# Optimization experiments

Measured on AMD Instinct MI355X. Metric: run time of the kernel, lower is better.

## Reference

```python
import jax, jax.numpy as jnp
import numpy as np

N_NODES = 100000
N_EDGES = 600000
IN_FEAT = 128
OUT_FEAT = 128
REL_NUM = 5


def setup_inputs() -> dict:
    key = jax.random.key(0)
    k = jax.random.split(key, 7)
    h = jax.random.normal(k[0], (N_NODES, IN_FEAT), dtype=jnp.float32)
    weight = jax.random.normal(k[1], (REL_NUM, IN_FEAT, OUT_FEAT), dtype=jnp.float32)
    W_0 = jax.random.normal(k[2], (IN_FEAT, OUT_FEAT), dtype=jnp.float32)
    norm = jax.random.uniform(k[3], (N_EDGES,), dtype=jnp.float32)
    src = jax.random.randint(k[4], (N_EDGES,), 0, N_NODES, dtype=jnp.int32)
    dst = jax.random.randint(k[5], (N_EDGES,), 0, N_NODES, dtype=jnp.int32)
    edge_id = jax.random.randint(k[6], (N_EDGES,), 0, REL_NUM, dtype=jnp.int32)
    return {"h": h, "weight": weight, "W_0": W_0, "norm": norm,
            "src": src, "dst": dst, "edge_id": edge_id}


def reference(h, weight, W_0, norm, src, dst, edge_id):
    # Per-edge msg = h[src] @ weight[edge_id] * norm.
    # Equivalent, efficient form: transform all nodes by every relation weight
    # once (R is small), then gather per edge instead of materializing an
    # [E, in, out] weight tensor.
    all_h = jnp.einsum('ni,rio->rno', h, weight)          # [R, N, out]
    msg = all_h[edge_id, src] * norm[:, None]             # [E, out]
    h_sum = jax.ops.segment_sum(msg, dst, num_segments=h.shape[0])  # [N, out]
    out = jax.nn.relu(h @ W_0 + h_sum)                    # [N, out]
    return out
```

## Files before the change

kernel.cpp:

```cpp
#include <hip/hip_runtime.h>
#include <hip/hip_bf16.h>


#define NN   100000
#define NE   600000
#define FEAT 128
#define RNUM 5
#define CAP  32
#define KC   24

#define SCAT_B 2344
#define BT_B   384

typedef __attribute__((ext_vector_type(8))) short short8;
typedef __attribute__((ext_vector_type(4))) float float4v;

static __device__ __forceinline__ unsigned short f2bf(float x) {
  union { float f; unsigned u; } v; v.f = x;
  unsigned r = v.u + 0x7FFFu + ((v.u >> 16) & 1u);
  return (unsigned short)(r >> 16);
}

__global__ void k_prep(const int* __restrict__ src, const int* __restrict__ dst,
                       const int* __restrict__ eid, const float* __restrict__ norm,
                       const float* __restrict__ weight, const float* __restrict__ W0,
                       int* __restrict__ cnt, int2* __restrict__ s_edge,
                       unsigned short* __restrict__ Bt) {
  int bid = blockIdx.x;
  if (bid < SCAT_B) {
    int e = bid * 256 + threadIdx.x;
    if (e < NE) {
      int d = dst[e];
      int p = atomicAdd(&cnt[d], 1);
      if (p < CAP) {
        union { float f; int i; } nb; nb.f = norm[e];
        s_edge[(size_t)d * CAP + p] = make_int2(src[e] | (eid[e] << 20), nb.i);
      }
    }
  } else {
    int u = (bid - SCAT_B) * 256 + threadIdx.x;
    if (u < FEAT * KC * 32) {
      int j = u & 7, g = u >> 3;
      int ln = g & 63, n0 = (g >> 6) & 7, c = g >> 9;
      int o = n0 * 16 + (ln & 15);
      int k = c * 32 + ((ln >> 4) << 3) + j;
      float v = (k < 640) ? weight[(k >> 7) * 16384 + (k & 127) * 128 + o]
                          : W0[(k - 640) * 128 + o];
      Bt[u] = f2bf(v);
    }
  }
}

static __device__ __forceinline__ void accum_edge(float acc[RNUM][4], int ex,
                                                  int ey, float4v v) {
  union { int i; float f; } nb; nb.i = ey;
  int r = ex >> 20;
  float nm[RNUM];
#pragma unroll
  for (int rr = 0; rr < RNUM; ++rr) nm[rr] = (r == rr) ? nb.f : 0.f;
#pragma unroll
  for (int rr = 0; rr < RNUM; ++rr)
#pragma unroll
    for (int i = 0; i < 4; ++i) acc[rr][i] += nm[rr] * v[i];
}

__global__ __launch_bounds__(512, 6) void k_fused(
    const float* __restrict__ h, const int* __restrict__ cnt,
    const int2* __restrict__ s_edge, const unsigned short* __restrict__ Bt,
    float* __restrict__ out) {
  __shared__ uint4 Atile[2 * KC * 64];
  int tid = threadIdx.x;
  int wv = tid >> 6, lane = tid & 63;
  int base = blockIdx.x * 32;
  uint4* Aw = Atile + (wv >> 2) * (KC * 64);
  uint2* Aw2 = (uint2*)Aw;
  const float4v* hf4 = (const float4v*)h;

  int g2 = lane >> 5, t2 = lane & 31;
  int cB = t2 >> 3, kk = (t2 >> 1) & 3, par = t2 & 1;
#pragma unroll 1
  for (int pp = 0; pp < 2; ++pp) {
    int node = base + wv * 4 + pp * 2 + g2;
    int row = (wv & 3) * 4 + pp * 2 + g2;
    int glen = cnt[node]; if (glen > CAP) glen = CAP;
    const int4* ep4 = (const int4*)(s_edge + (size_t)node * CAP);
    float4v idf = hf4[(size_t)node * 32 + t2];
    float acc[RNUM][4] = {};
    int npair = glen >> 1;
    int4 d = (glen > 0) ? ep4[0] : make_int4(0, 0, 0, 0);
    for (int p = 0; p < npair; ++p) {
      int4 dn = ep4[p + 1];
      float4v v0 = hf4[(size_t)(d.x & 0xFFFFF) * 32 + t2];
      float4v v1 = hf4[(size_t)(d.z & 0xFFFFF) * 32 + t2];
      accum_edge(acc, d.x, d.y, v0);
      accum_edge(acc, d.z, d.w, v1);
      d = dn;
    }
    if (glen & 1) {
      float4v v = hf4[(size_t)(d.x & 0xFFFFF) * 32 + t2];
      accum_edge(acc, d.x, d.y, v);
    }
#pragma unroll
    for (int rr = 0; rr < RNUM; ++rr) {
      int c = rr * 4 + cB;
      uint2 pk;
      pk.x = (unsigned)f2bf(acc[rr][0]) | ((unsigned)f2bf(acc[rr][1]) << 16);
      pk.y = (unsigned)f2bf(acc[rr][2]) | ((unsigned)f2bf(acc[rr][3]) << 16);
      int sidx = c * 64 + kk * 16 + (row ^ ((c * 4 + kk) & 7));
      Aw2[sidx * 2 + par] = pk;
    }
    {
      int c = 20 + cB;
      uint2 idv;
      idv.x = (unsigned)f2bf(idf[0]) | ((unsigned)f2bf(idf[1]) << 16);
      idv.y = (unsigned)f2bf(idf[2]) | ((unsigned)f2bf(idf[3]) << 16);
      int sidx = c * 64 + kk * 16 + (row ^ ((c * 4 + kk) & 7));
      Aw2[sidx * 2 + par] = idv;
    }
  }
  __syncthreads();

  int m = lane & 15, qq = lane >> 4;
  float4v cacc[2];
  cacc[0] = (float4v){0.f, 0.f, 0.f, 0.f};
  cacc[1] = (float4v){0.f, 0.f, 0.f, 0.f};
#pragma unroll
  for (int c = 0; c < KC; ++c) {
    int sx = qq * 16 + (m ^ ((c * 4 + qq) & 7));
    short8 af0 = *(const short8*)&Atile[c * 64 + sx];
    short8 af1 = *(const short8*)&Atile[KC * 64 + c * 64 + sx];
    short8 bf  = *(const short8*)&Bt[((c * 8 + wv) * 64 + lane) * 8];
    cacc[0] = __builtin_amdgcn_mfma_f32_16x16x32_bf16(af0, bf, cacc[0], 0, 0, 0);
    cacc[1] = __builtin_amdgcn_mfma_f32_16x16x32_bf16(af1, bf, cacc[1], 0, 0, 0);
  }

  __syncthreads();
  float* Cs = (float*)Atile;
#pragma unroll
  for (int tt = 0; tt < 2; ++tt)
#pragma unroll
    for (int r = 0; r < 4; ++r) {
      float v = cacc[tt][r];
      Cs[(tt * 16 + qq * 4 + r) * 132 + wv * 16 + m] = v > 0.f ? v : 0.f;
    }
  __syncthreads();
  int r0 = tid >> 4, c0 = (tid & 15) * 8;
  float4v w0 = *(const float4v*)&Cs[r0 * 132 + c0];
  float4v w1 = *(const float4v*)&Cs[r0 * 132 + c0 + 4];
  float* op = out + (size_t)(base + r0) * FEAT + c0;
  *(float4v*)op = w0;
  *(float4v*)(op + 4) = w1;
}

__global__ void k_slow_mm(const float* __restrict__ h, const float* __restrict__ W0,
                          float* __restrict__ out) {
  __shared__ float hn[128];
  int n = blockIdx.x, t = threadIdx.x;
  hn[t] = h[(size_t)n * 128 + t];
  __syncthreads();
  float a = 0.f;
  for (int i = 0; i < 128; ++i) a += hn[i] * W0[i * 128 + t];
  out[(size_t)n * 128 + t] = a;
}
__global__ void k_slow_edge(const float* __restrict__ h, const float* __restrict__ weight,
                            const float* __restrict__ norm, const int* __restrict__ src,
                            const int* __restrict__ dst, const int* __restrict__ eid,
                            float* __restrict__ out) {
  __shared__ float hs[128];
  int e = blockIdx.x, t = threadIdx.x;
  hs[t] = h[(size_t)src[e] * 128 + t];
  __syncthreads();
  const float* W = weight + (size_t)eid[e] * 16384;
  float a = 0.f;
  for (int i = 0; i < 128; ++i) a += hs[i] * W[i * 128 + t];
  atomicAdd(&out[(size_t)dst[e] * 128 + t], a * norm[e]);
}
__global__ void k_slow_relu(float* out) {
  int i = blockIdx.x * 256 + threadIdx.x;
  if (i < NN * FEAT) out[i] = fmaxf(out[i], 0.f);
}

extern "C" void kernel_launch(void* const* d_in, const int* in_sizes, int n_in,
                              void* d_out, int out_size, void* d_ws, size_t ws_size,
                              hipStream_t stream) {
  const float* h      = (const float*)d_in[0];
  const float* weight = (const float*)d_in[1];
  const float* W0     = (const float*)d_in[2];
  const float* norm   = (const float*)d_in[3];
  const int*   src    = (const int*)d_in[4];
  const int*   dst    = (const int*)d_in[5];
  const int*   eid    = (const int*)d_in[6];
  float* out = (float*)d_out;

  char* ws = (char*)d_ws;
  size_t off = 0;
  auto wsalloc = [&](size_t bytes) -> char* {
    char* p = ws + off;
    off += (bytes + 255) & ~(size_t)255;
    return p;
  };
  unsigned short* Bt  = (unsigned short*)wsalloc((size_t)FEAT * KC * 32 * 2);
  int*   cnt      = (int*)wsalloc((size_t)NN * 4);
  int2*  s_edge   = (int2*)wsalloc((size_t)NN * CAP * 8 + 256);

  if (ws_size >= off) {
    hipMemsetAsync(cnt, 0, (size_t)NN * 4, stream);
    k_prep <<<SCAT_B + BT_B, 256, 0, stream>>>(src, dst, eid, norm, weight,
                                               W0, cnt, s_edge, Bt);
    k_fused<<<NN / 32, 512, 0, stream>>>(h, cnt, s_edge, Bt, out);
  } else {
    k_slow_mm  <<<NN, 128, 0, stream>>>(h, W0, out);
    k_slow_edge<<<NE, 128, 0, stream>>>(h, weight, norm, src, dst, eid, out);
    k_slow_relu<<<(NN * FEAT + 255) / 256, 256, 0, stream>>>(out);
  }
}
```

Measured before the change: 203.8 us.

## Fuse memset, prep and fused compute into one cooperative persistent kernel

Replaces the memset plus two launches with a single cooperative kernel. It zeroes the counters and fills the weight tile, then does a grid sync, the edge scatter, another grid sync, and finally processes node tiles through a persistent loop driven by an atomic tile counter. The aim is to remove launch gaps and kernel-boundary drains, at the cost of two grid-wide barriers and a lower occupancy bound (4 waves per SIMD instead of 6) with a fixed 512-block grid. If the cooperative launch fails, it falls back to the old path.

```diff
diff --git a/kernel.cpp b/kernel.cpp
--- a/kernel.cpp
+++ b/kernel.cpp
@@ -1,5 +1,6 @@
 #include <hip/hip_runtime.h>
 #include <hip/hip_bf16.h>
+#include <hip/hip_cooperative_groups.h>
 
 
 #define NN   100000
@@ -8,6 +9,9 @@
 #define RNUM 5
 #define CAP  32
 #define KC   24
+#define NTILE (NN / 32)
+#define CGRID 512
+#define GSTRIDE (CGRID * 512)
 
 #define SCAT_B 2344
 #define BT_B   384
@@ -19,6 +23,149 @@
   union { float f; unsigned u; } v; v.f = x;
   unsigned r = v.u + 0x7FFFu + ((v.u >> 16) & 1u);
   return (unsigned short)(r >> 16);
+}
+
+static __device__ __forceinline__ void bt_fill(int u, const float* __restrict__ weight,
+                                               const float* __restrict__ W0,
+                                               unsigned short* __restrict__ Bt) {
+  int j = u & 7, g = u >> 3;
+  int ln = g & 63, n0 = (g >> 6) & 7, c = g >> 9;
+  int o = n0 * 16 + (ln & 15);
+  int k = c * 32 + ((ln >> 4) << 3) + j;
+  float v = (k < 640) ? weight[(k >> 7) * 16384 + (k & 127) * 128 + o]
+                      : W0[(k - 640) * 128 + o];
+  Bt[u] = f2bf(v);
+}
+
+static __device__ __forceinline__ void accum_edge(float acc[RNUM][4], int ex,
+                                                  int ey, float4v v) {
+  union { int i; float f; } nb; nb.i = ey;
+  int r = ex >> 20;
+  float nm[RNUM];
+#pragma unroll
+  for (int rr = 0; rr < RNUM; ++rr) nm[rr] = (r == rr) ? nb.f : 0.f;
+#pragma unroll
+  for (int rr = 0; rr < RNUM; ++rr)
+#pragma unroll
+    for (int i = 0; i < 4; ++i) acc[rr][i] += nm[rr] * v[i];
+}
+
+__global__ __launch_bounds__(512, 4) void k_all(
+    const float* __restrict__ h, const int* __restrict__ src,
+    const int* __restrict__ dst, const int* __restrict__ eid,
+    const float* __restrict__ norm, const float* __restrict__ weight,
+    const float* __restrict__ W0, int* __restrict__ cnt,
+    int2* __restrict__ s_edge, unsigned short* __restrict__ Bt,
+    float* __restrict__ out) {
+  namespace cg = cooperative_groups;
+  cg::grid_group grid = cg::this_grid();
+  __shared__ uint4 Atile[2 * KC * 64];
+  __shared__ int tsh;
+  int tid = threadIdx.x;
+  int gtid = blockIdx.x * 512 + tid;
+
+  if (gtid <= NN) cnt[gtid] = 0;
+  if (gtid < FEAT * KC * 32) bt_fill(gtid, weight, W0, Bt);
+  grid.sync();
+
+  for (int e = gtid; e < NE; e += GSTRIDE) {
+    int d = dst[e];
+    int p = atomicAdd(&cnt[d], 1);
+    if (p < CAP) {
+      union { float f; int i; } nb; nb.f = norm[e];
+      s_edge[(size_t)d * CAP + p] = make_int2(src[e] | (eid[e] << 20), nb.i);
+    }
+  }
+  grid.sync();
+
+  int wv = tid >> 6, lane = tid & 63;
+  int g2 = lane >> 5, t2 = lane & 31;
+  int cB = t2 >> 3, kk = (t2 >> 1) & 3, par = t2 & 1;
+  int m = lane & 15, qq = lane >> 4;
+  uint4* Aw = Atile + (wv >> 2) * (KC * 64);
+  uint2* Aw2 = (uint2*)Aw;
+  const float4v* hf4 = (const float4v*)h;
+
+  for (;;) {
+    __syncthreads();
+    if (tid == 0) tsh = atomicAdd(&cnt[NN], 1);
+    __syncthreads();
+    int tile = tsh;
+    if (tile >= NTILE) break;
+    int base = tile * 32;
+
+#pragma unroll 1
+    for (int pp = 0; pp < 2; ++pp) {
+      int node = base + wv * 4 + pp * 2 + g2;
+      int row = (wv & 3) * 4 + pp * 2 + g2;
+      int glen = cnt[node]; if (glen > CAP) glen = CAP;
+      const int4* ep4 = (const int4*)(s_edge + (size_t)node * CAP);
+      float4v idf = hf4[(size_t)node * 32 + t2];
+      float acc[RNUM][4] = {};
+      int npair = glen >> 1;
+      int4 d = (glen > 0) ? ep4[0] : make_int4(0, 0, 0, 0);
+      for (int p = 0; p < npair; ++p) {
+        int4 dn = ep4[p + 1];
+        float4v v0 = hf4[(size_t)(d.x & 0xFFFFF) * 32 + t2];
+        float4v v1 = hf4[(size_t)(d.z & 0xFFFFF) * 32 + t2];
+        accum_edge(acc, d.x, d.y, v0);
+        accum_edge(acc, d.z, d.w, v1);
+        d = dn;
+      }
+      if (glen & 1) {
+        float4v v = hf4[(size_t)(d.x & 0xFFFFF) * 32 + t2];
+        accum_edge(acc, d.x, d.y, v);
+      }
+#pragma unroll
+      for (int rr = 0; rr < RNUM; ++rr) {
+        int c = rr * 4 + cB;
+        uint2 pk;
+        pk.x = (unsigned)f2bf(acc[rr][0]) | ((unsigned)f2bf(acc[rr][1]) << 16);
+        pk.y = (unsigned)f2bf(acc[rr][2]) | ((unsigned)f2bf(acc[rr][3]) << 16);
+        int sidx = c * 64 + kk * 16 + (row ^ ((c * 4 + kk) & 7));
+        Aw2[sidx * 2 + par] = pk;
+      }
+      {
+        int c = 20 + cB;
+        uint2 idv;
+        idv.x = (unsigned)f2bf(idf[0]) | ((unsigned)f2bf(idf[1]) << 16);
+        idv.y = (unsigned)f2bf(idf[2]) | ((unsigned)f2bf(idf[3]) << 16);
+        int sidx = c * 64 + kk * 16 + (row ^ ((c * 4 + kk) & 7));
+        Aw2[sidx * 2 + par] = idv;
+      }
+    }
+    __syncthreads();
+
+    float4v cacc[2];
+    cacc[0] = (float4v){0.f, 0.f, 0.f, 0.f};
+    cacc[1] = (float4v){0.f, 0.f, 0.f, 0.f};
+#pragma unroll
+    for (int c = 0; c < KC; ++c) {
+      int sx = qq * 16 + (m ^ ((c * 4 + qq) & 7));
+      short8 af0 = *(const short8*)&Atile[c * 64 + sx];
+      short8 af1 = *(const short8*)&Atile[KC * 64 + c * 64 + sx];
+      short8 bf  = *(const short8*)&Bt[((c * 8 + wv) * 64 + lane) * 8];
+      cacc[0] = __builtin_amdgcn_mfma_f32_16x16x32_bf16(af0, bf, cacc[0], 0, 0, 0);
+      cacc[1] = __builtin_amdgcn_mfma_f32_16x16x32_bf16(af1, bf, cacc[1], 0, 0, 0);
+    }
+
+    __syncthreads();
+    float* Cs = (float*)Atile;
+#pragma unroll
+    for (int tt = 0; tt < 2; ++tt)
+#pragma unroll
+      for (int r = 0; r < 4; ++r) {
+        float v = cacc[tt][r];
+        Cs[(tt * 16 + qq * 4 + r) * 132 + wv * 16 + m] = v > 0.f ? v : 0.f;
+      }
+    __syncthreads();
+    int r0 = tid >> 4, c0 = (tid & 15) * 8;
+    float4v w0 = *(const float4v*)&Cs[r0 * 132 + c0];
+    float4v w1 = *(const float4v*)&Cs[r0 * 132 + c0 + 4];
+    float* op = out + (size_t)(base + r0) * FEAT + c0;
+    *(float4v*)op = w0;
+    *(float4v*)(op + 4) = w1;
+  }
 }
 
 __global__ void k_prep(const int* __restrict__ src, const int* __restrict__ dst,
@@ -39,29 +186,8 @@
     }
   } else {
     int u = (bid - SCAT_B) * 256 + threadIdx.x;
-    if (u < FEAT * KC * 32) {
-      int j = u & 7, g = u >> 3;
-      int ln = g & 63, n0 = (g >> 6) & 7, c = g >> 9;
-      int o = n0 * 16 + (ln & 15);
-      int k = c * 32 + ((ln >> 4) << 3) + j;
-      float v = (k < 640) ? weight[(k >> 7) * 16384 + (k & 127) * 128 + o]
-                          : W0[(k - 640) * 128 + o];
-      Bt[u] = f2bf(v);
-    }
-  }
-}
-
-static __device__ __forceinline__ void accum_edge(float acc[RNUM][4], int ex,
-                                                  int ey, float4v v) {
-  union { int i; float f; } nb; nb.i = ey;
-  int r = ex >> 20;
-  float nm[RNUM];
-#pragma unroll
-  for (int rr = 0; rr < RNUM; ++rr) nm[rr] = (r == rr) ? nb.f : 0.f;
-#pragma unroll
-  for (int rr = 0; rr < RNUM; ++rr)
-#pragma unroll
-    for (int i = 0; i < 4; ++i) acc[rr][i] += nm[rr] * v[i];
+    if (u < FEAT * KC * 32) bt_fill(u, weight, W0, Bt);
+  }
 }
 
 __global__ __launch_bounds__(512, 6) void k_fused(
@@ -75,7 +201,6 @@
   uint4* Aw = Atile + (wv >> 2) * (KC * 64);
   uint2* Aw2 = (uint2*)Aw;
   const float4v* hf4 = (const float4v*)h;
-
   int g2 = lane >> 5, t2 = lane & 31;
   int cB = t2 >> 3, kk = (t2 >> 1) & 3, par = t2 & 1;
 #pragma unroll 1
@@ -119,7 +244,6 @@
     }
   }
   __syncthreads();
-
   int m = lane & 15, qq = lane >> 4;
   float4v cacc[2];
   cacc[0] = (float4v){0.f, 0.f, 0.f, 0.f};
@@ -133,7 +257,6 @@
     cacc[0] = __builtin_amdgcn_mfma_f32_16x16x32_bf16(af0, bf, cacc[0], 0, 0, 0);
     cacc[1] = __builtin_amdgcn_mfma_f32_16x16x32_bf16(af1, bf, cacc[1], 0, 0, 0);
   }
-
   __syncthreads();
   float* Cs = (float*)Atile;
 #pragma unroll
@@ -200,14 +323,21 @@
     return p;
   };
   unsigned short* Bt  = (unsigned short*)wsalloc((size_t)FEAT * KC * 32 * 2);
-  int*   cnt      = (int*)wsalloc((size_t)NN * 4);
+  int*   cnt      = (int*)wsalloc((size_t)(NN + 256) * 4);
   int2*  s_edge   = (int2*)wsalloc((size_t)NN * CAP * 8 + 256);
 
   if (ws_size >= off) {
-    hipMemsetAsync(cnt, 0, (size_t)NN * 4, stream);
-    k_prep <<<SCAT_B + BT_B, 256, 0, stream>>>(src, dst, eid, norm, weight,
-                                               W0, cnt, s_edge, Bt);
-    k_fused<<<NN / 32, 512, 0, stream>>>(h, cnt, s_edge, Bt, out);
+    void* args[] = {(void*)&h, (void*)&src, (void*)&dst, (void*)&eid,
+                    (void*)&norm, (void*)&weight, (void*)&W0, (void*)&cnt,
+                    (void*)&s_edge, (void*)&Bt, (void*)&out};
+    hipError_t rc = hipLaunchCooperativeKernel(
+        reinterpret_cast<void*>(k_all), dim3(CGRID), dim3(512), args, 0, stream);
+    if (rc != hipSuccess) {
+      hipMemsetAsync(cnt, 0, (size_t)NN * 4, stream);
+      k_prep <<<SCAT_B + BT_B, 256, 0, stream>>>(src, dst, eid, norm, weight,
+                                                 W0, cnt, s_edge, Bt);
+      k_fused<<<NN / 32, 512, 0, stream>>>(h, cnt, s_edge, Bt, out);
+    }
   } else {
     k_slow_mm  <<<NN, 128, 0, stream>>>(h, W0, out);
     k_slow_edge<<<NE, 128, 0, stream>>>(h, weight, norm, src, dst, eid, out);
```

Result: slower. 351.7 us (+72.6%).

## Gather four nodes per wave at once with 16 lanes each, 32-byte loads

Applied to the files above, without the earlier changes.

The aggregation phase no longer loops twice over two nodes per wave with 32 lanes each. It now handles four nodes per wave in one pass, with 16 lanes per node and each lane loading two float4 (32 bytes) per neighbor row. The aim is more independent gather streams in flight per wave and removal of the serial outer loop, so memory latency is better hidden. In exchange, each lane keeps twice as many accumulators (40 floats), which adds register pressure under launch_bounds(512,6).

```diff
diff --git a/kernel.cpp b/kernel.cpp
--- a/kernel.cpp
+++ b/kernel.cpp
@@ -51,17 +51,20 @@
   }
 }
 
-static __device__ __forceinline__ void accum_edge(float acc[RNUM][4], int ex,
-                                                  int ey, float4v v) {
+static __device__ __forceinline__ void accum_edge8(float acc[RNUM][8], int ex,
+                                                   int ey, float4v va, float4v vb) {
   union { int i; float f; } nb; nb.i = ey;
   int r = ex >> 20;
   float nm[RNUM];
 #pragma unroll
   for (int rr = 0; rr < RNUM; ++rr) nm[rr] = (r == rr) ? nb.f : 0.f;
 #pragma unroll
-  for (int rr = 0; rr < RNUM; ++rr)
-#pragma unroll
-    for (int i = 0; i < 4; ++i) acc[rr][i] += nm[rr] * v[i];
+  for (int rr = 0; rr < RNUM; ++rr) {
+#pragma unroll
+    for (int i = 0; i < 4; ++i) acc[rr][i] += nm[rr] * va[i];
+#pragma unroll
+    for (int i = 0; i < 4; ++i) acc[rr][4 + i] += nm[rr] * vb[i];
+  }
 }
 
 __global__ __launch_bounds__(512, 6) void k_fused(
@@ -71,52 +74,54 @@
   __shared__ uint4 Atile[2 * KC * 64];
   int tid = threadIdx.x;
   int wv = tid >> 6, lane = tid & 63;
+  int g = lane >> 4, t = lane & 15;
   int base = blockIdx.x * 32;
+  int node = base + wv * 4 + g;
+  int row = (wv & 3) * 4 + g;
   uint4* Aw = Atile + (wv >> 2) * (KC * 64);
-  uint2* Aw2 = (uint2*)Aw;
   const float4v* hf4 = (const float4v*)h;
 
-  int g2 = lane >> 5, t2 = lane & 31;
-  int cB = t2 >> 3, kk = (t2 >> 1) & 3, par = t2 & 1;
-#pragma unroll 1
-  for (int pp = 0; pp < 2; ++pp) {
-    int node = base + wv * 4 + pp * 2 + g2;
-    int row = (wv & 3) * 4 + pp * 2 + g2;
-    int glen = cnt[node]; if (glen > CAP) glen = CAP;
-    const int4* ep4 = (const int4*)(s_edge + (size_t)node * CAP);
-    float4v idf = hf4[(size_t)node * 32 + t2];
-    float acc[RNUM][4] = {};
-    int npair = glen >> 1;
-    int4 d = (glen > 0) ? ep4[0] : make_int4(0, 0, 0, 0);
-    for (int p = 0; p < npair; ++p) {
-      int4 dn = ep4[p + 1];
-      float4v v0 = hf4[(size_t)(d.x & 0xFFFFF) * 32 + t2];
-      float4v v1 = hf4[(size_t)(d.z & 0xFFFFF) * 32 + t2];
-      accum_edge(acc, d.x, d.y, v0);
-      accum_edge(acc, d.z, d.w, v1);
-      d = dn;
-    }
-    if (glen & 1) {
-      float4v v = hf4[(size_t)(d.x & 0xFFFFF) * 32 + t2];
-      accum_edge(acc, d.x, d.y, v);
-    }
-#pragma unroll
-    for (int rr = 0; rr < RNUM; ++rr) {
-      int c = rr * 4 + cB;
-      uint2 pk;
-      pk.x = (unsigned)f2bf(acc[rr][0]) | ((unsigned)f2bf(acc[rr][1]) << 16);
-      pk.y = (unsigned)f2bf(acc[rr][2]) | ((unsigned)f2bf(acc[rr][3]) << 16);
-      int sidx = c * 64 + kk * 16 + (row ^ ((c * 4 + kk) & 7));
-      Aw2[sidx * 2 + par] = pk;
-    }
-    {
-      int c = 20 + cB;
-      uint2 idv;
-      idv.x = (unsigned)f2bf(idf[0]) | ((unsigned)f2bf(idf[1]) << 16);
-      idv.y = (unsigned)f2bf(idf[2]) | ((unsigned)f2bf(idf[3]) << 16);
-      int sidx = c * 64 + kk * 16 + (row ^ ((c * 4 + kk) & 7));
-      Aw2[sidx * 2 + par] = idv;
-    }
+  int glen = cnt[node]; if (glen > CAP) glen = CAP;
+  const int4* ep4 = (const int4*)(s_edge + (size_t)node * CAP);
+  float4v ida = hf4[(size_t)node * 32 + t * 2];
+  float4v idb = hf4[(size_t)node * 32 + t * 2 + 1];
+  float acc[RNUM][8] = {};
+  int npair = glen >> 1;
+  int4 d = (glen > 0) ? ep4[0] : make_int4(0, 0, 0, 0);
+  for (int p = 0; p < npair; ++p) {
+    int4 dn = ep4[p + 1];
+    size_t r0 = (size_t)(d.x & 0xFFFFF) * 32 + t * 2;
+    size_t r1 = (size_t)(d.z & 0xFFFFF) * 32 + t * 2;
+    float4v v0a = hf4[r0], v0b = hf4[r0 + 1];
+    float4v v1a = hf4[r1], v1b = hf4[r1 + 1];
+    accum_edge8(acc, d.x, d.y, v0a, v0b);
+    accum_edge8(acc, d.z, d.w, v1a, v1b);
+    d = dn;
+  }
+  if (glen & 1) {
+    size_t r0 = (size_t)(d.x & 0xFFFFF) * 32 + t * 2;
+    float4v va = hf4[r0], vb = hf4[r0 + 1];
+    accum_edge8(acc, d.x, d.y, va, vb);
+  }
+  int q = t & 3, cb = t >> 2;
+#pragma unroll
+  for (int rr = 0; rr < RNUM; ++rr) {
+    int c = rr * 4 + cb;
+    uint4 pk;
+    pk.x = (unsigned)f2bf(acc[rr][0]) | ((unsigned)f2bf(acc[rr][1]) << 16);
+    pk.y = (unsigned)f2bf(acc[rr][2]) | ((unsigned)f2bf(acc[rr][3]) << 16);
+    pk.z = (unsigned)f2bf(acc[rr][4]) | ((unsigned)f2bf(acc[rr][5]) << 16);
+    pk.w = (unsigned)f2bf(acc[rr][6]) | ((unsigned)f2bf(acc[rr][7]) << 16);
+    Aw[c * 64 + q * 16 + (row ^ ((c * 4 + q) & 7))] = pk;
+  }
+  {
+    int c = 20 + cb;
+    uint4 idv;
+    idv.x = (unsigned)f2bf(ida[0]) | ((unsigned)f2bf(ida[1]) << 16);
+    idv.y = (unsigned)f2bf(ida[2]) | ((unsigned)f2bf(ida[3]) << 16);
+    idv.z = (unsigned)f2bf(idb[0]) | ((unsigned)f2bf(idb[1]) << 16);
+    idv.w = (unsigned)f2bf(idb[2]) | ((unsigned)f2bf(idb[3]) << 16);
+    Aw[c * 64 + q * 16 + (row ^ ((c * 4 + q) & 7))] = idv;
   }
   __syncthreads();
 
```

New measurement: 213.3 us. +4.7%, slower.
